# Kernel optimization log

Hardware: AMD Instinct MI355X
Metric: run time of the kernel (lower is better)

Reference implementation:

```python
import jax, jax.numpy as jnp
import numpy as np

DIM = 512
H = 8
HS = DIM // H
SCALES = [25, 12, 7]
ATTN_SCALE = HS ** -0.5
EPS = 1e-5


def _ln(x, g, b):
    m = jnp.mean(x, axis=-1, keepdims=True)
    v = jnp.mean((x - m) ** 2, axis=-1, keepdims=True)
    return (x - m) * jax.lax.rsqrt(v + EPS) * g + b


def setup_inputs() -> dict:
    key = jax.random.key(0)
    ks = jax.random.split(key, 12)
    B, T, J, C = 64, 64, 25, DIM
    w = lambda k, s: jax.random.normal(k, s, dtype=jnp.float32) * 0.02
    return {
        "src": jax.random.normal(ks[0], (B, T, J, C), dtype=jnp.float32),
        "spatial_relation": jax.random.normal(ks[1], (B, T, J, J, 2), dtype=jnp.float32),
        "ln1_g": jnp.ones((C,), jnp.float32),
        "ln1_b": jnp.zeros((C,), jnp.float32),
        "Wq": w(ks[2], (3, C, C)),
        "Wk": w(ks[3], (3, C, C)),
        "Wv": w(ks[4], (3, C, C)),
        "pool0_fc1_w": w(ks[5], (C, 2 * C)),
        "pool0_fc1_b": jnp.zeros((2 * C,), jnp.float32),
        "pool0_fc2_w": w(ks[6], (2 * C, SCALES[1])),
        "pool0_fc2_b": jnp.zeros((SCALES[1],), jnp.float32),
        "pool1_fc1_w": w(ks[7], (C, 2 * C)),
        "pool1_fc1_b": jnp.zeros((2 * C,), jnp.float32),
        "pool1_fc2_w": w(ks[8], (2 * C, SCALES[2])),
        "pool1_fc2_b": jnp.zeros((SCALES[2],), jnp.float32),
    }


def reference(src, spatial_relation, ln1_g, ln1_b, Wq, Wk, Wv,
              pool0_fc1_w, pool0_fc1_b, pool0_fc2_w, pool0_fc2_b,
              pool1_fc1_w, pool1_fc1_b, pool1_fc2_w, pool1_fc2_b):
    # NOTE: in the original torch module, the relation-bias terms (R_qk, R_conv,
    # attn_R_qurt) and spatial_relation_emb are computed but never added to the
    # attention logits, so they do not affect the output; faithful output math below.
    B, T, J, C = src.shape
    x = src.reshape(B * T, J, C)
    g_feat = x  # global (query) features, stay at J nodes
    l_feat = x  # local (key/value) features, get pooled
    pools = [
        (pool0_fc1_w, pool0_fc1_b, pool0_fc2_w, pool0_fc2_b),
        (pool1_fc1_w, pool1_fc1_b, pool1_fc2_w, pool1_fc2_b),
    ]
    outs = []
    for i in range(len(SCALES)):
        qn = _ln(g_feat, ln1_g, ln1_b)
        kn = _ln(l_feat, ln1_g, ln1_b)
        q = (qn @ Wq[i]).reshape(B * T, J, H, HS)
        k = (kn @ Wk[i]).reshape(B * T, -1, H, HS)
        v = (kn @ Wv[i]).reshape(B * T, -1, H, HS)
        logits = jnp.einsum('bnhd,bmhd->bhnm', q, k) * ATTN_SCALE
        a = jax.nn.softmax(logits, axis=-1)
        o = jnp.einsum('bhnm,bmhd->bnhd', a, v).reshape(B * T, J, C)
        outs.append(g_feat + o)
        if i < len(SCALES) - 1:
            f1w, f1b, f2w, f2b = pools[i]
            h = jax.nn.gelu(l_feat @ f1w + f1b, approximate=False)
            S = jax.nn.softmax(h @ f2w + f2b, axis=-1)  # (BT, Ni, Ni+1)
            l_feat = jnp.einsum('bns,bnc->bsc', S, l_feat)
    return jnp.mean(jnp.stack(outs, axis=-1), axis=-1)
```

## Files before the change

kernel.cpp:

```cpp
#include <hip/hip_runtime.h>

typedef unsigned short u16;
typedef unsigned int   u32;
typedef _Float16 f16;
typedef __attribute__((ext_vector_type(8))) unsigned short u16x8;
typedef __attribute__((ext_vector_type(8))) _Float16 f16x8;
typedef __attribute__((ext_vector_type(4))) float f32x4;

__device__ __forceinline__ u16 f2h(float f) {
  f16 h = (f16)f;
  return __builtin_bit_cast(u16, h);
}
__device__ __forceinline__ float h2f(u16 u) {
  return (float)__builtin_bit_cast(f16, u);
}

__global__ __launch_bounds__(256) void prep_w(const float* __restrict__ Wq,
    const float* __restrict__ Wk, const float* __restrict__ Wv,
    const float* __restrict__ f0, const float* __restrict__ f1,
    u16* __restrict__ wt) {
  int t = blockIdx.x * 256 + threadIdx.x;
  float v;
  if (t < 786432) {
    int i = t >> 18, r = t & 262143, n = r >> 9, k = r & 511;
    v = Wq[(size_t)(i << 18) + k * 512 + n];
  } else if (t < 2359296) {
    int r = t - 786432, i = r >> 19, r2 = r & 524287;
    int n = (r2 >> 9) & 511, k = r2 & 511;
    v = ((r2 >> 18) ? Wv : Wk)[(size_t)(i << 18) + k * 512 + n];
  } else if (t < 2883584) {
    int r = t - 2359296, n = r >> 9, k = r & 511;
    v = f0[(size_t)k * 1024 + n];
  } else {
    int r = t - 2883584, n = r >> 9, k = r & 511;
    v = f1[(size_t)k * 1024 + n];
  }
  wt[t] = f2h(v);
}

__global__ __launch_bounds__(256) void ln_f32(const float* __restrict__ x,
    const float* __restrict__ g, const float* __restrict__ bta,
    u16* __restrict__ xn, u16* __restrict__ xb) {
  int row = (blockIdx.x << 2) + (threadIdx.x >> 6);
  int lane = threadIdx.x & 63;
  const float* xr = x + (size_t)row * 512 + (lane << 3);
  float4 a = *(const float4*)xr;
  float4 c = *(const float4*)(xr + 4);
  float v[8] = {a.x, a.y, a.z, a.w, c.x, c.y, c.z, c.w};
  float s = 0.f, s2 = 0.f;
#pragma unroll
  for (int j = 0; j < 8; ++j) { s += v[j]; s2 += v[j] * v[j]; }
  for (int off = 32; off; off >>= 1) { s += __shfl_xor(s, off); s2 += __shfl_xor(s2, off); }
  float mean = s * (1.f / 512.f);
  float var = s2 * (1.f / 512.f) - mean * mean;
  float rs = rsqrtf(var + 1e-5f);
  const float* gp = g + (lane << 3);
  const float* bp = bta + (lane << 3);
  u16x8 pb, pn;
#pragma unroll
  for (int j = 0; j < 8; ++j) {
    pb[j] = f2h(v[j]);
    pn[j] = f2h((v[j] - mean) * rs * gp[j] + bp[j]);
  }
  *(u16x8*)(xb + (size_t)row * 512 + (lane << 3)) = pb;
  *(u16x8*)(xn + (size_t)row * 512 + (lane << 3)) = pn;
}

__global__ __launch_bounds__(256) void ln_b16(const u16* __restrict__ xin,
    const float* __restrict__ g, const float* __restrict__ bta,
    u16* __restrict__ xout) {
  int row = (blockIdx.x << 2) + (threadIdx.x >> 6);
  int lane = threadIdx.x & 63;
  f16x8 u = *(const f16x8*)(xin + (size_t)row * 512 + (lane << 3));
  float v[8];
#pragma unroll
  for (int j = 0; j < 8; ++j) v[j] = (float)u[j];
  float s = 0.f, s2 = 0.f;
#pragma unroll
  for (int j = 0; j < 8; ++j) { s += v[j]; s2 += v[j] * v[j]; }
  for (int off = 32; off; off >>= 1) { s += __shfl_xor(s, off); s2 += __shfl_xor(s2, off); }
  float mean = s * (1.f / 512.f);
  float var = s2 * (1.f / 512.f) - mean * mean;
  float rs = rsqrtf(var + 1e-5f);
  const float* gp = g + (lane << 3);
  const float* bp = bta + (lane << 3);
  u16x8 pn;
#pragma unroll
  for (int j = 0; j < 8; ++j) pn[j] = f2h((v[j] - mean) * rs * gp[j] + bp[j]);
  *(u16x8*)(xout + (size_t)row * 512 + (lane << 3)) = pn;
}

template <bool GELU>
__global__ __launch_bounds__(256, 2) void gemm_bt(const u16* __restrict__ A,
    const u16* __restrict__ Bt, u16* __restrict__ C,
    const float* __restrict__ bias, int M, int N) {
  __shared__ __align__(16) u16 As[128 * 64];
  __shared__ __align__(16) u16 Bs[128 * 64];
  int tid = threadIdx.x;
  int w = tid >> 6, lane = tid & 63;
  int m0 = blockIdx.y << 7, n0 = blockIdx.x << 7;
  int wm = (w & 1) << 6, wn = (w >> 1) << 6;
  f32x4 acc[4][4] = {};
  const int r_off = lane >> 3;
  const int k_off = (lane & 7) << 3;
  for (int kt = 0; kt < 8; ++kt) {
    __syncthreads();
#pragma unroll
    for (int j = 0; j < 4; ++j) {
      int q = (w << 2) + j;
      const u16* gA = A + (size_t)(m0 + (q << 3) + r_off) * 512 + (kt << 6) + k_off;
      __builtin_amdgcn_global_load_lds(
          (const __attribute__((address_space(1))) u32*)gA,
          (__attribute__((address_space(3))) u32*)(As + (q << 9)), 16, 0, 0);
      const u16* gB = Bt + (size_t)(n0 + (q << 3) + r_off) * 512 + (kt << 6) + k_off;
      __builtin_amdgcn_global_load_lds(
          (const __attribute__((address_space(1))) u32*)gB,
          (__attribute__((address_space(3))) u32*)(Bs + (q << 9)), 16, 0, 0);
    }
    asm volatile("s_waitcnt vmcnt(0)" ::: "memory");
    __syncthreads();
#pragma unroll
    for (int kk = 0; kk < 2; ++kk) {
      int ko = (kk << 5) + ((lane >> 4) << 3);
      f16x8 af[4], bfr[4];
#pragma unroll
      for (int mi = 0; mi < 4; ++mi)
        af[mi] = *(const f16x8*)(As + (wm + (mi << 4) + (lane & 15)) * 64 + ko);
#pragma unroll
      for (int ni = 0; ni < 4; ++ni)
        bfr[ni] = *(const f16x8*)(Bs + (wn + (ni << 4) + (lane & 15)) * 64 + ko);
#pragma unroll
      for (int mi = 0; mi < 4; ++mi)
#pragma unroll
        for (int ni = 0; ni < 4; ++ni)
          acc[mi][ni] = __builtin_amdgcn_mfma_f32_16x16x32_f16(af[mi], bfr[ni], acc[mi][ni], 0, 0, 0);
    }
  }
  int cr = (lane >> 4) << 2, cc = lane & 15;
#pragma unroll
  for (int mi = 0; mi < 4; ++mi) {
#pragma unroll
    for (int ni = 0; ni < 4; ++ni) {
      int col = n0 + wn + (ni << 4) + cc;
      float bv = 0.f;
      if (GELU) bv = bias[col];
#pragma unroll
      for (int j = 0; j < 4; ++j) {
        int row = m0 + wm + (mi << 4) + cr + j;
        float v = acc[mi][ni][j];
        if (GELU) { v += bv; v = 0.5f * v * (1.f + erff(v * 0.70710678118f)); }
        C[(size_t)row * N + col] = f2h(v);
      }
    }
  }
}

template <int NKV, bool INIT>
__global__ __launch_bounds__(512, 2) void attn(const u16* __restrict__ Q,
    const u16* __restrict__ KV, const u16* __restrict__ xb, float* __restrict__ out) {
  __shared__ __align__(16) u16 KVl[NKV * 1024];
  int b = blockIdx.x, tid = threadIdx.x;
  const u16* kvb = KV + (size_t)b * (NKV * 1024);
  for (int e = tid * 8; e < NKV * 1024; e += 4096)
    *(u16x8*)(KVl + e) = *(const u16x8*)(kvb + e);
  __syncthreads();
  int h = tid >> 6, r = tid & 63, n = r >> 1, half = r & 1;
  if (n < 25) {
    int dbase = (h << 6) + (half << 5);
    const u16* qr = Q + (size_t)(b * 25 + n) * 512 + dbase;
    f16x8 q8[4];
#pragma unroll
    for (int i = 0; i < 4; ++i) q8[i] = *(const f16x8*)(qr + (i << 3));
    float s[NKV];
    float mx = -1e30f;
#pragma unroll
    for (int m = 0; m < NKV; ++m) {
      const u16* kr = KVl + m * 1024 + dbase;
      float p = 0.f;
#pragma unroll
      for (int i = 0; i < 4; ++i) {
        f16x8 kv = *(const f16x8*)(kr + (i << 3));
#pragma unroll
        for (int j = 0; j < 8; ++j) p += (float)q8[i][j] * (float)kv[j];
      }
      float d = p + __shfl_xor(p, 1);
      s[m] = d * 0.125f;
      mx = fmaxf(mx, s[m]);
    }
    float sum = 0.f;
#pragma unroll
    for (int m = 0; m < NKV; ++m) { s[m] = __expf(s[m] - mx); sum += s[m]; }
    float o[32] = {};
#pragma unroll
    for (int m = 0; m < NKV; ++m) {
      float a = s[m];
      const u16* vr = KVl + m * 1024 + 512 + dbase;
#pragma unroll
      for (int i = 0; i < 4; ++i) {
        f16x8 vv = *(const f16x8*)(vr + (i << 3));
#pragma unroll
        for (int j = 0; j < 8; ++j) o[i * 8 + j] += a * (float)vv[j];
      }
    }
    float sc = (1.f / sum) * (1.f / 3.f);
    float* orow = out + (size_t)(b * 25 + n) * 512 + dbase;
    if (INIT) {
      const u16* xrow = xb + (size_t)(b * 25 + n) * 512 + dbase;
#pragma unroll
      for (int i = 0; i < 4; ++i) {
        f16x8 xv = *(const f16x8*)(xrow + (i << 3));
#pragma unroll
        for (int j = 0; j < 8; j += 4) {
          float4 rr;
          rr.x = o[i * 8 + j + 0] * sc + (float)xv[j + 0];
          rr.y = o[i * 8 + j + 1] * sc + (float)xv[j + 1];
          rr.z = o[i * 8 + j + 2] * sc + (float)xv[j + 2];
          rr.w = o[i * 8 + j + 3] * sc + (float)xv[j + 3];
          *(float4*)(orow + i * 8 + j) = rr;
        }
      }
    } else {
#pragma unroll
      for (int i = 0; i < 8; ++i) {
        float4 pv = *(const float4*)(orow + i * 4);
        float4 rr;
        rr.x = o[i * 4 + 0] * sc + pv.x;
        rr.y = o[i * 4 + 1] * sc + pv.y;
        rr.z = o[i * 4 + 2] * sc + pv.z;
        rr.w = o[i * 4 + 3] * sc + pv.w;
        *(float4*)(orow + i * 4) = rr;
      }
    }
  }
}

template <int NIN, int NOUT>
__global__ __launch_bounds__(256) void pool(const u16* __restrict__ h,
    const u16* __restrict__ lf, const float* __restrict__ w2,
    const float* __restrict__ b2, u16* __restrict__ lout) {
  __shared__ __align__(16) float W2l[1024 * NOUT];
  __shared__ __align__(16) u16 Xl[NIN * 512];
  __shared__ __align__(16) float Sl[NIN * NOUT];
  int b = blockIdx.x, tid = threadIdx.x;
  for (int e = tid; e < 1024 * NOUT; e += 256) W2l[e] = w2[e];
  for (int e = tid * 8; e < NIN * 512; e += 2048)
    *(u16x8*)(Xl + e) = *(const u16x8*)(lf + (size_t)b * NIN * 512 + e);
  __syncthreads();
  if (tid < NIN * 8) {
    int nn = tid >> 3, sub = tid & 7;
    float p[NOUT] = {};
    const u16* hr = h + (size_t)(b * NIN + nn) * 1024;
    for (int cc = 0; cc < 128; ++cc) {
      int c = sub + (cc << 3);
      float hv = h2f(hr[c]);
#pragma unroll
      for (int s2 = 0; s2 < NOUT; ++s2) p[s2] += hv * W2l[c * NOUT + s2];
    }
#pragma unroll
    for (int s2 = 0; s2 < NOUT; ++s2) {
      p[s2] += __shfl_down(p[s2], 4, 8);
      p[s2] += __shfl_down(p[s2], 2, 8);
      p[s2] += __shfl_down(p[s2], 1, 8);
    }
    if (sub == 0) {
      float mx = -1e30f;
#pragma unroll
      for (int s2 = 0; s2 < NOUT; ++s2) { p[s2] += b2[s2]; mx = fmaxf(mx, p[s2]); }
      float sum = 0.f;
#pragma unroll
      for (int s2 = 0; s2 < NOUT; ++s2) { p[s2] = __expf(p[s2] - mx); sum += p[s2]; }
      float inv = 1.f / sum;
#pragma unroll
      for (int s2 = 0; s2 < NOUT; ++s2) Sl[nn * NOUT + s2] = p[s2] * inv;
    }
  }
  __syncthreads();
  int c0 = tid << 1;
#pragma unroll
  for (int s2 = 0; s2 < NOUT; ++s2) {
    float a0 = 0.f, a1 = 0.f;
#pragma unroll
    for (int nn = 0; nn < NIN; ++nn) {
      float wv = Sl[nn * NOUT + s2];
      a0 += wv * h2f(Xl[nn * 512 + c0]);
      a1 += wv * h2f(Xl[nn * 512 + c0 + 1]);
    }
    u32 pk = (u32)f2h(a0) | ((u32)f2h(a1) << 16);
    *(u32*)(lout + (size_t)(b * NOUT + s2) * 512 + c0) = pk;
  }
}

extern "C" void kernel_launch(void* const* d_in, const int* in_sizes, int n_in,
                              void* d_out, int out_size, void* d_ws, size_t ws_size,
                              hipStream_t stream) {
  const float* src = (const float*)d_in[0];
  const float* g    = (const float*)d_in[2];
  const float* bt   = (const float*)d_in[3];
  const float* Wq   = (const float*)d_in[4];
  const float* Wk   = (const float*)d_in[5];
  const float* Wv   = (const float*)d_in[6];
  const float* f0w  = (const float*)d_in[7];
  const float* f0b  = (const float*)d_in[8];
  const float* f0w2 = (const float*)d_in[9];
  const float* f0b2 = (const float*)d_in[10];
  const float* f1w  = (const float*)d_in[11];
  const float* f1b  = (const float*)d_in[12];
  const float* f1w2 = (const float*)d_in[13];
  const float* f1b2 = (const float*)d_in[14];
  float* out = (float*)d_out;
  char* ws = (char*)d_ws;

  u16* wt  = (u16*)(ws + 0);
  u16* xn  = (u16*)(ws + 6815744);
  u16* xb  = (u16*)(ws + 111673344);
  u16* qb  = (u16*)(ws + 216530944);
  u16* B1  = (u16*)(ws + 321388544);
  u16* l1  = (u16*)(ws + 426246144);
  u16* kn1 = (u16*)(ws + 476577792);
  u16* l2  = qb;
  u16* kn2 = qb + 14680064;

  prep_w<<<13312, 256, 0, stream>>>(Wq, Wk, Wv, f0w, f1w, wt);
  ln_f32<<<25600, 256, 0, stream>>>(src, g, bt, xn, xb);

  gemm_bt<false><<<dim3(4, 800), 256, 0, stream>>>(xn, wt, qb, nullptr, 102400, 512);
  for (int s = 0; s < 2; ++s) {
    size_t ro = (size_t)s * 51200;
    gemm_bt<false><<<dim3(8, 400), 256, 0, stream>>>(xn + ro * 512, wt + 786432, B1, nullptr, 51200, 1024);
    attn<25, true><<<2048, 512, 0, stream>>>(qb + ro * 512, B1, xb + ro * 512, out + ro * 512);
  }

  for (int s = 0; s < 2; ++s) {
    size_t ro = (size_t)s * 51200;
    gemm_bt<true><<<dim3(8, 400), 256, 0, stream>>>(xb + ro * 512, wt + 2359296, B1, f0b, 51200, 1024);
    pool<25, 12><<<2048, 256, 0, stream>>>(B1, xb + ro * 512, f0w2, f0b2, l1 + (size_t)s * 2048 * 12 * 512);
  }
  ln_b16<<<12288, 256, 0, stream>>>(l1, g, bt, kn1);

  gemm_bt<false><<<dim3(4, 800), 256, 0, stream>>>(xn, wt + 262144, qb, nullptr, 102400, 512);
  gemm_bt<false><<<dim3(8, 384), 256, 0, stream>>>(kn1, wt + 786432 + 524288, B1, nullptr, 49152, 1024);
  attn<12, false><<<4096, 512, 0, stream>>>(qb, B1, nullptr, out);

  gemm_bt<true><<<dim3(8, 384), 256, 0, stream>>>(l1, wt + 2883584, B1, f1b, 49152, 1024);
  pool<12, 7><<<4096, 256, 0, stream>>>(B1, l1, f1w2, f1b2, l2);
  ln_b16<<<7168, 256, 0, stream>>>(l2, g, bt, kn2);

  gemm_bt<false><<<dim3(8, 224), 256, 0, stream>>>(kn2, wt + 786432 + 1048576, B1, nullptr, 28672, 1024);
  gemm_bt<false><<<dim3(4, 800), 256, 0, stream>>>(xn, wt + 524288, qb, nullptr, 102400, 512);
  attn<7, false><<<4096, 512, 0, stream>>>(qb, B1, nullptr, out);
}
```

Measured before the change: 1.810 ms.

## Make attention persistent over 8 batches with double-buffered async KV loads to LDS

```diff
diff --git a/kernel.cpp b/kernel.cpp
--- a/kernel.cpp
+++ b/kernel.cpp
@@ -155,82 +155,104 @@
   }
 }
 
-template <int NKV, bool INIT>
-__global__ __launch_bounds__(512, 2) void attn(const u16* __restrict__ Q,
+template <int NKV, bool INIT, int MINW>
+__global__ __launch_bounds__(512, MINW) void attn(const u16* __restrict__ Q,
     const u16* __restrict__ KV, const u16* __restrict__ xb, float* __restrict__ out) {
-  __shared__ __align__(16) u16 KVl[NKV * 1024];
-  int b = blockIdx.x, tid = threadIdx.x;
-  const u16* kvb = KV + (size_t)b * (NKV * 1024);
-  for (int e = tid * 8; e < NKV * 1024; e += 4096)
-    *(u16x8*)(KVl + e) = *(const u16x8*)(kvb + e);
+  constexpr int G = 8;
+  constexpr int ELEMS = NKV * 1024;
+  __shared__ __align__(16) u16 KVl[2][ELEMS];
+  int tid = threadIdx.x;
+  int b0 = blockIdx.x * G;
+  int h = tid >> 6, r = tid & 63, n = r >> 1, half = r & 1;
+  int dbase = (h << 6) + (half << 5);
+  {
+    const u16* src = KV + (size_t)b0 * ELEMS;
+    for (int e = tid * 8; e < ELEMS; e += 4096)
+      __builtin_amdgcn_global_load_lds(
+          (const __attribute__((address_space(1))) u32*)(src + e),
+          (__attribute__((address_space(3))) u32*)(KVl[0] + e), 16, 0, 0);
+  }
+  asm volatile("s_waitcnt vmcnt(0)" ::: "memory");
   __syncthreads();
-  int h = tid >> 6, r = tid & 63, n = r >> 1, half = r & 1;
-  if (n < 25) {
-    int dbase = (h << 6) + (half << 5);
-    const u16* qr = Q + (size_t)(b * 25 + n) * 512 + dbase;
-    f16x8 q8[4];
-#pragma unroll
-    for (int i = 0; i < 4; ++i) q8[i] = *(const f16x8*)(qr + (i << 3));
-    float s[NKV];
-    float mx = -1e30f;
-#pragma unroll
-    for (int m = 0; m < NKV; ++m) {
-      const u16* kr = KVl + m * 1024 + dbase;
-      float p = 0.f;
-#pragma unroll
-      for (int i = 0; i < 4; ++i) {
-        f16x8 kv = *(const f16x8*)(kr + (i << 3));
-#pragma unroll
-        for (int j = 0; j < 8; ++j) p += (float)q8[i][j] * (float)kv[j];
+  for (int t = 0; t < G; ++t) {
+    const u16* KVc = KVl[t & 1];
+    if (t + 1 < G) {
+      const u16* src = KV + (size_t)(b0 + t + 1) * ELEMS;
+      u16* dst = KVl[(t + 1) & 1];
+      for (int e = tid * 8; e < ELEMS; e += 4096)
+        __builtin_amdgcn_global_load_lds(
+            (const __attribute__((address_space(1))) u32*)(src + e),
+            (__attribute__((address_space(3))) u32*)(dst + e), 16, 0, 0);
+    }
+    int b = b0 + t;
+    if (n < 25) {
+      const u16* qr = Q + (size_t)(b * 25 + n) * 512 + dbase;
+      f16x8 q8[4];
+#pragma unroll
+      for (int i = 0; i < 4; ++i) q8[i] = *(const f16x8*)(qr + (i << 3));
+      float s[NKV];
+      float mx = -1e30f;
+#pragma unroll
+      for (int m = 0; m < NKV; ++m) {
+        const u16* kr = KVc + m * 1024 + dbase;
+        float p = 0.f;
+#pragma unroll
+        for (int i = 0; i < 4; ++i) {
+          f16x8 kv = *(const f16x8*)(kr + (i << 3));
+#pragma unroll
+          for (int j = 0; j < 8; ++j) p += (float)q8[i][j] * (float)kv[j];
+        }
+        float d = p + __shfl_xor(p, 1);
+        s[m] = d * 0.125f;
+        mx = fmaxf(mx, s[m]);
       }
-      float d = p + __shfl_xor(p, 1);
-      s[m] = d * 0.125f;
-      mx = fmaxf(mx, s[m]);
-    }
-    float sum = 0.f;
-#pragma unroll
-    for (int m = 0; m < NKV; ++m) { s[m] = __expf(s[m] - mx); sum += s[m]; }
-    float o[32] = {};
-#pragma unroll
-    for (int m = 0; m < NKV; ++m) {
-      float a = s[m];
-      const u16* vr = KVl + m * 1024 + 512 + dbase;
-#pragma unroll
-      for (int i = 0; i < 4; ++i) {
-        f16x8 vv = *(const f16x8*)(vr + (i << 3));
-#pragma unroll
-        for (int j = 0; j < 8; ++j) o[i * 8 + j] += a * (float)vv[j];
-      }
-    }
-    float sc = (1.f / sum) * (1.f / 3.f);
-    float* orow = out + (size_t)(b * 25 + n) * 512 + dbase;
-    if (INIT) {
-      const u16* xrow = xb + (size_t)(b * 25 + n) * 512 + dbase;
-#pragma unroll
-      for (int i = 0; i < 4; ++i) {
-        f16x8 xv = *(const f16x8*)(xrow + (i << 3));
-#pragma unroll
-        for (int j = 0; j < 8; j += 4) {
-          float4 rr;
-          rr.x = o[i * 8 + j + 0] * sc + (float)xv[j + 0];
-          rr.y = o[i * 8 + j + 1] * sc + (float)xv[j + 1];
-          rr.z = o[i * 8 + j + 2] * sc + (float)xv[j + 2];
-          rr.w = o[i * 8 + j + 3] * sc + (float)xv[j + 3];
-          *(float4*)(orow + i * 8 + j) = rr;
+      float sum = 0.f;
+#pragma unroll
+      for (int m = 0; m < NKV; ++m) { s[m] = __expf(s[m] - mx); sum += s[m]; }
+      float o[32] = {};
+#pragma unroll
+      for (int m = 0; m < NKV; ++m) {
+        float a = s[m];
+        const u16* vr = KVc + m * 1024 + 512 + dbase;
+#pragma unroll
+        for (int i = 0; i < 4; ++i) {
+          f16x8 vv = *(const f16x8*)(vr + (i << 3));
+#pragma unroll
+          for (int j = 0; j < 8; ++j) o[i * 8 + j] += a * (float)vv[j];
         }
       }
-    } else {
-#pragma unroll
-      for (int i = 0; i < 8; ++i) {
-        float4 pv = *(const float4*)(orow + i * 4);
-        float4 rr;
-        rr.x = o[i * 4 + 0] * sc + pv.x;
-        rr.y = o[i * 4 + 1] * sc + pv.y;
-        rr.z = o[i * 4 + 2] * sc + pv.z;
-        rr.w = o[i * 4 + 3] * sc + pv.w;
-        *(float4*)(orow + i * 4) = rr;
+      float sc = (1.f / sum) * (1.f / 3.f);
+      float* orow = out + (size_t)(b * 25 + n) * 512 + dbase;
+      if (INIT) {
+        const u16* xrow = xb + (size_t)(b * 25 + n) * 512 + dbase;
+#pragma unroll
+        for (int i = 0; i < 4; ++i) {
+          f16x8 xv = *(const f16x8*)(xrow + (i << 3));
+#pragma unroll
+          for (int j = 0; j < 8; j += 4) {
+            float4 rr;
+            rr.x = o[i * 8 + j + 0] * sc + (float)xv[j + 0];
+            rr.y = o[i * 8 + j + 1] * sc + (float)xv[j + 1];
+            rr.z = o[i * 8 + j + 2] * sc + (float)xv[j + 2];
+            rr.w = o[i * 8 + j + 3] * sc + (float)xv[j + 3];
+            *(float4*)(orow + i * 8 + j) = rr;
+          }
+        }
+      } else {
+#pragma unroll
+        for (int i = 0; i < 8; ++i) {
+          float4 pv = *(const float4*)(orow + i * 4);
+          float4 rr;
+          rr.x = o[i * 4 + 0] * sc + pv.x;
+          rr.y = o[i * 4 + 1] * sc + pv.y;
+          rr.z = o[i * 4 + 2] * sc + pv.z;
+          rr.w = o[i * 4 + 3] * sc + pv.w;
+          *(float4*)(orow + i * 4) = rr;
+        }
       }
     }
+    asm volatile("s_waitcnt vmcnt(0)" ::: "memory");
+    __syncthreads();
   }
 }
 
@@ -327,7 +349,7 @@
   for (int s = 0; s < 2; ++s) {
     size_t ro = (size_t)s * 51200;
     gemm_bt<false><<<dim3(8, 400), 256, 0, stream>>>(xn + ro * 512, wt + 786432, B1, nullptr, 51200, 1024);
-    attn<25, true><<<2048, 512, 0, stream>>>(qb + ro * 512, B1, xb + ro * 512, out + ro * 512);
+    attn<25, true, 1><<<256, 512, 0, stream>>>(qb + ro * 512, B1, xb + ro * 512, out + ro * 512);
   }
 
   for (int s = 0; s < 2; ++s) {
@@ -339,7 +361,7 @@
 
   gemm_bt<false><<<dim3(4, 800), 256, 0, stream>>>(xn, wt + 262144, qb, nullptr, 102400, 512);
   gemm_bt<false><<<dim3(8, 384), 256, 0, stream>>>(kn1, wt + 786432 + 524288, B1, nullptr, 49152, 1024);
-  attn<12, false><<<4096, 512, 0, stream>>>(qb, B1, nullptr, out);
+  attn<12, false, 2><<<512, 512, 0, stream>>>(qb, B1, nullptr, out);
 
   gemm_bt<true><<<dim3(8, 384), 256, 0, stream>>>(l1, wt + 2883584, B1, f1b, 49152, 1024);
   pool<12, 7><<<4096, 256, 0, stream>>>(B1, l1, f1w2, f1b2, l2);
@@ -347,5 +369,5 @@
 
   gemm_bt<false><<<dim3(8, 224), 256, 0, stream>>>(kn2, wt + 786432 + 1048576, B1, nullptr, 28672, 1024);
   gemm_bt<false><<<dim3(4, 800), 256, 0, stream>>>(xn, wt + 524288, qb, nullptr, 102400, 512);
-  attn<7, false><<<4096, 512, 0, stream>>>(qb, B1, nullptr, out);
-}
+  attn<7, false, 2><<<512, 512, 0, stream>>>(qb, B1, nullptr, out);
+}
```

Measured after the change: 1.773 ms. 1.02x faster.
